# Kernel optimization log

Hardware: AMD Instinct MI355X
Metric: run time of the kernel (lower is better)

## Reference

```python
import jax, jax.numpy as jnp
import numpy as np

B, H, W, C = 2, 64, 64, 512
EPS = 1e-3  # keras BatchNormalization default epsilon


def _bn(x, g, b, m, v):
    # inference-mode batch norm over the last axis
    return (x - m) * jax.lax.rsqrt(v + EPS) * g + b


def setup_inputs() -> dict:
    key = jax.random.key(0)
    ks = jax.random.split(key, 12)
    C2 = C // 2

    def he(k, shape, fan_in):
        return jax.random.normal(k, shape, jnp.float32) * np.float32(np.sqrt(2.0 / fan_in))

    def bn_params(k, n):
        k1, k2, k3, k4 = jax.random.split(k, 4)
        g = 1.0 + 0.1 * jax.random.normal(k1, (n,), jnp.float32)
        b = 0.1 * jax.random.normal(k2, (n,), jnp.float32)
        m = 0.1 * jax.random.normal(k3, (n,), jnp.float32)
        v = jax.random.uniform(k4, (n,), jnp.float32, 0.5, 1.5)
        return g, b, m, v

    g1, b1, m1, v1 = bn_params(ks[1], 1)
    g2, b2, m2, v2 = bn_params(ks[2], C2)
    g3, b3, m3, v3 = bn_params(ks[3], C2)
    g4, b4, m4, v4 = bn_params(ks[4], 1)
    g5, b5, m5, v5 = bn_params(ks[5], C)

    return {
        "x": jax.random.normal(ks[0], (B, H, W, C), jnp.float32),
        # edge_aggregation_func: Dense(1) over the 4-neighbor axis
        "w_ea": he(ks[6], (4, 1), 4), "b_ea": jnp.zeros((1,), jnp.float32),
        "g1": g1, "b1": b1, "m1": m1, "v1": v1,
        # vertex_update_func: Dense(C//2) over 2C features
        "w_vu": he(ks[7], (2 * C, C2), 2 * C), "b_vu": jnp.zeros((C2,), jnp.float32),
        "g2": g2, "b2": b2, "m2": m2, "v2": v2,
        # edge_update_func: Dense(C//2) over 2C features
        "w_eu": he(ks[8], (2 * C, C2), 2 * C), "b_eu": jnp.zeros((C2,), jnp.float32),
        "g3": g3, "b3": b3, "m3": m3, "v3": v3,
        # update_edge_reduce_func: Dense(1) over the 4-neighbor axis
        "w_er": he(ks[9], (4, 1), 4), "b_er": jnp.zeros((1,), jnp.float32),
        "g4": g4, "b4": b4, "m4": m4, "v4": v4,
        # final 1x1 conv (no bias): [C + C//2, C]
        "w_fc": he(ks[10], (C + C2, C), C + C2),
        "g5": g5, "b5": b5, "m5": m5, "v5": v5,
    }


def reference(x, w_ea, b_ea, g1, b1, m1, v1,
              w_vu, b_vu, g2, b2, m2, v2,
              w_eu, b_eu, g3, b3, m3, v3,
              w_er, b_er, g4, b4, m4, v4,
              w_fc, g5, b5, m5, v5):
    # 4-neighbor cyclic-shift edges: [B,H,W,C,4] (H+1, H-1, W+1, W-1 rolls)
    neigh = jnp.stack([
        jnp.roll(x, 1, axis=1), jnp.roll(x, -1, axis=1),
        jnp.roll(x, 1, axis=2), jnp.roll(x, -1, axis=2)], axis=-1)
    edge = neigh * x[..., None]                                   # [B,H,W,C,4]

    # edge aggregation: Dense(1) over neighbor axis + BN(1) + ReLU
    agg = jax.nn.relu(_bn(jnp.einsum('bhwcn,no->bhwco', edge, w_ea) + b_ea,
                          g1, b1, m1, v1))[..., 0]                # [B,H,W,C]

    # vertex update: Dense(C/2) on concat([vertex, agg]) + BN + ReLU
    cat_v = jnp.concatenate([x, agg], axis=-1)                    # [B,H,W,2C]
    uv = jax.nn.relu(_bn(cat_v @ w_vu + b_vu, g2, b2, m2, v2))    # [B,H,W,C/2]

    # edge update: Dense(C/2) on concat([vertex x4, edge]) along channel
    vert4 = jnp.broadcast_to(x[..., None], edge.shape)            # [B,H,W,C,4]
    cat_e = jnp.concatenate([vert4, edge], axis=3)                # [B,H,W,2C,4]
    ue = jax.nn.relu(_bn(jnp.einsum('bhwcn,cd->bhwnd', cat_e, w_eu) + b_eu,
                         g3, b3, m3, v3))                          # [B,H,W,4,C/2]

    # reduce updated edges over neighbor axis: Dense(1) + BN(1) + ReLU
    ur = jax.nn.relu(_bn(jnp.einsum('bhwnd,no->bhwdo', ue, w_er) + b_er,
                         g4, b4, m4, v4))[..., 0]                 # [B,H,W,C/2]

    update_feature = uv * ur                                      # [B,H,W,C/2]

    # final aggregation: 1x1 conv (no bias) on concat([x, update]) + BN + ReLU
    out = jax.nn.relu(_bn(jnp.concatenate([x, update_feature], axis=-1) @ w_fc,
                          g5, b5, m5, v5))                         # [B,H,W,C]
    return out
```

## Files before the change

kernel.cpp:

```cpp
#include <hip/hip_runtime.h>
#include <stdint.h>


typedef __attribute__((ext_vector_type(8))) short bf16x8;
typedef __attribute__((ext_vector_type(4))) float f32x4;

#define EPS_BN 1e-3f

__device__ __forceinline__ short f2bf(float f) {
    union { float f; unsigned u; } cv;
    cv.f = f;
    unsigned r = cv.u + 0x7fffu + ((cv.u >> 16) & 1u);
    return (short)(r >> 16);
}
__device__ __forceinline__ float bf2f(short s) {
    union { unsigned u; float f; } cv;
    cv.u = ((unsigned)(unsigned short)s) << 16;
    return cv.f;
}


__device__ __forceinline__ void pack_one(const float* __restrict__ W, short* __restrict__ out,
                                         int K, int Ncol, int lb, int tid) {
    int i = lb * 256 + tid;
    int lane = i & 63, tile = i >> 6;
    int ktiles = K >> 5;
    int nt = tile / ktiles, kt = tile - nt * ktiles;
    int kbase = (kt << 5) + ((lane >> 4) << 3);
    int col = (nt << 4) + (lane & 15);
    bf16x8 v;
    #pragma unroll
    for (int j = 0; j < 8; ++j) v[j] = f2bf(W[(kbase + j) * Ncol + col]);
    ((bf16x8*)out)[(tile << 6) + lane] = v;
}

__global__ __launch_bounds__(256) void k_front(
    const float* __restrict__ x,
    const float* w_ea, const float* b_ea,
    const float* g1, const float* b1, const float* m1, const float* v1,
    const float* w_vu, const float* w_eu, const float* w_fc,
    const float* b_vu, const float* g2, const float* b2_, const float* m2, const float* v2,
    const float* b_eu, const float* g3, const float* b3, const float* m3, const float* v3,
    const float* w_er, const float* b_er,
    const float* g4, const float* b4, const float* m4, const float* v4,
    const float* g5, const float* b5, const float* m5, const float* v5,
    short* __restrict__ xb, short* __restrict__ agg,
    short* __restrict__ prodD, short* __restrict__ prodR,
    short* BpVu, short* BpEu, short* BpFc, float* P)
{
    int blk = blockIdx.x, t = threadIdx.x;
    if (blk >= 2048) {
        int b = blk - 2048;
        if (b < 128)      { pack_one(w_vu, BpVu, 1024, 256, b, t); }
        else if (b < 256) { pack_one(w_eu, BpEu, 1024, 256, b - 128, t); }
        else if (b < 448) { pack_one(w_fc, BpFc,  768, 512, b - 256, t); }
        else {
            for (int u = t; u < 512; u += 256) {
                float a5 = g5[u] * rsqrtf(v5[u] + EPS_BN);
                P[1032 + u] = a5;
                P[1544 + u] = b5[u] - m5[u] * a5;
            }
            {
                float a2 = g2[t] * rsqrtf(v2[t] + EPS_BN);
                P[8 + t]   = a2;
                P[264 + t] = (b_vu[t] - m2[t]) * a2 + b2_[t];
                float a3 = g3[t] * rsqrtf(v3[t] + EPS_BN);
                P[520 + t] = a3;
                P[776 + t] = (b_eu[t] - m3[t]) * a3 + b3[t];
            }
            if (t < 4) {
                P[2056 + t] = w_ea[t];
                P[2060 + t] = w_er[t];
            }
            if (t == 0) {
                float a4 = g4[0] * rsqrtf(v4[0] + EPS_BN);
                P[2] = a4;
                P[3] = (b_er[0] - m4[0]) * a4 + b4[0];
                float a1l = g1[0] * rsqrtf(v1[0] + EPS_BN);
                P[0] = a1l;
                P[1] = (b_ea[0] - m1[0]) * a1l + b1[0];
            }
        }
        return;
    }

    float a1 = g1[0] * rsqrtf(v1[0] + EPS_BN);
    float c1 = (b_ea[0] - m1[0]) * a1 + b1[0];
    float w0 = w_ea[0], w1 = w_ea[1], w2 = w_ea[2], w3 = w_ea[3];

    int idx = blk * 256 + t;
    int n = idx >> 6;
    int ci = idx & 63;
    int bh = n >> 6, h = bh & 63, w = n & 63;
    int bhb = bh & ~63;
    int rowU = ((bhb + ((h + 63) & 63)) << 6) + w;
    int rowD = ((bhb + ((h + 1) & 63)) << 6) + w;
    int rowL = (bh << 6) + ((w + 63) & 63);
    int rowR = (bh << 6) + ((w + 1) & 63);

    const f32x4* xv = (const f32x4*)x;
    int c4 = ci << 1;
    f32x4 vc[2], vU[2], vD[2], vL[2], vR[2];
    #pragma unroll
    for (int h2 = 0; h2 < 2; ++h2) {
        vc[h2] = xv[(n    << 7) + c4 + h2];
        vU[h2] = xv[(rowU << 7) + c4 + h2];
        vD[h2] = xv[(rowD << 7) + c4 + h2];
        vL[h2] = xv[(rowL << 7) + c4 + h2];
        vR[h2] = xv[(rowR << 7) + c4 + h2];
    }

    bf16x8 ob, xbv, pD, pR;
    #pragma unroll
    for (int h2 = 0; h2 < 2; ++h2) {
        #pragma unroll
        for (int j = 0; j < 4; ++j) {
            int e = h2 * 4 + j;
            float xc = vc[h2][j];
            float eU = xc * vU[h2][j], eD = xc * vD[h2][j];
            float eL = xc * vL[h2][j], eR = xc * vR[h2][j];
            float S = w0 * eU + w1 * eD + w2 * eL + w3 * eR;
            ob[e]  = f2bf(fmaxf(fmaf(a1, S, c1), 0.f));
            xbv[e] = f2bf(xc);
            pD[e] = f2bf(eD); pR[e] = f2bf(eR);
        }
    }
    int o = (n << 6) + ci;
    ((bf16x8*)agg)[o] = ob;
    ((bf16x8*)xb)[o] = xbv;
    ((bf16x8*)prodD)[o] = pD;
    ((bf16x8*)prodR)[o] = pR;
}

__global__ __launch_bounds__(256) void k_gemm_mid(
    const short* __restrict__ xb, const short* __restrict__ agg,
    const short* __restrict__ prodD, const short* __restrict__ prodR,
    const short* __restrict__ BpVu, const short* __restrict__ BpEu,
    const float* __restrict__ P,
    short* __restrict__ uvb, short* __restrict__ tvb,
    short* __restrict__ teDb, short* __restrict__ teRb)
{
    __shared__ __align__(16) short sA[2][32 * 64];
    int t = threadIdx.x, l = t & 63, w = t >> 6;
    int type = blockIdx.x & 3, rs = blockIdx.x >> 2;
    int r0 = rs << 5;

    const short* A0; const short* A1; int nchunk, ktbase;
    const bf16x8* Bp; short* Out;
    if (type == 0)      { A0 = xb;    A1 = agg;   nchunk = 16; Bp = (const bf16x8*)BpVu; ktbase = 0;  Out = uvb;  }
    else if (type == 1) { A0 = xb;    A1 = xb;    nchunk = 8;  Bp = (const bf16x8*)BpEu; ktbase = 0;  Out = tvb;  }
    else if (type == 2) { A0 = prodD; A1 = prodD; nchunk = 8;  Bp = (const bf16x8*)BpEu; ktbase = 16; Out = teDb; }
    else                { A0 = prodR; A1 = prodR; nchunk = 8;  Bp = (const bf16x8*)BpEu; ktbase = 16; Out = teRb; }

    int dr = t >> 3;
    int lcs = ((t & 7) ^ (dr & 7)) << 3;
    int srow = (r0 + dr) << 9;

    f32x4 acc[2][4];
    #pragma unroll
    for (int mi = 0; mi < 2; ++mi)
        #pragma unroll
        for (int nf = 0; nf < 4; ++nf) acc[mi][nf] = (f32x4){0.f, 0.f, 0.f, 0.f};

    bf16x8 g0 = *(const bf16x8*)(A0 + srow + lcs);

    int buf = 0;
    for (int kc = 0; kc < nchunk; ++kc) {
        ((bf16x8*)sA[buf])[t] = g0;
        __syncthreads();
        if (kc + 1 < nchunk) {
            int kn = kc + 1;
            const short* S = (kn < 8) ? A0 : A1;
            g0 = *(const bf16x8*)(S + srow + ((kn & 7) << 6) + lcs);
        }
        const short* Lb = sA[buf];
        #pragma unroll
        for (int kt = 0; kt < 2; ++kt) {
            bf16x8 af[2];
            #pragma unroll
            for (int mi = 0; mi < 2; ++mi) {
                int row = (mi << 4) + (l & 15);
                int lcolb = (kt << 6) + ((l >> 4) << 4);
                int addr = (row << 6) + ((lcolb ^ ((row & 7) << 4)) >> 1);
                af[mi] = *(const bf16x8*)(Lb + addr);
            }
            int kt32 = ktbase + (kc << 1) + kt;
            #pragma unroll
            for (int nf = 0; nf < 4; ++nf) {
                bf16x8 b = Bp[((((w << 2) + nf) << 5) + kt32) * 64 + l];
                #pragma unroll
                for (int mi = 0; mi < 2; ++mi)
                    acc[mi][nf] = __builtin_amdgcn_mfma_f32_16x16x32_bf16(af[mi], b, acc[mi][nf], 0, 0, 0);
            }
        }
        buf ^= 1;
    }

    #pragma unroll
    for (int nf = 0; nf < 4; ++nf) {
        int col = (w << 6) + (nf << 4) + (l & 15);
        float aa = P[8 + col], cc = P[264 + col];
        #pragma unroll
        for (int mi = 0; mi < 2; ++mi) {
            int rbase = r0 + (mi << 4) + ((l >> 4) << 2);
            #pragma unroll
            for (int j = 0; j < 4; ++j) {
                float v = acc[mi][nf][j];
                if (type == 0) v = fmaxf(fmaf(v, aa, cc), 0.f);
                Out[(rbase + j) * 256 + col] = f2bf(v);
            }
        }
    }
}

__global__ __launch_bounds__(256) void k_gemm_out(
    const short* __restrict__ xb,
    const short* __restrict__ tv, const short* __restrict__ teD,
    const short* __restrict__ teR, const short* __restrict__ uv,
    const short* __restrict__ BpFc, const float* __restrict__ P,
    float* __restrict__ out)
{
    __shared__ __align__(16) short sA[2][32 * 64];
    __shared__ __align__(16) short updL[4][32 * 64];
    int t = threadIdx.x, l = t & 63, w = t >> 6;
    int cq = blockIdx.x & 3, rs = blockIdx.x >> 2;
    int r0 = rs << 5;
    const bf16x8* Bp = (const bf16x8*)BpFc;

    int dr = t >> 3;
    int p8 = t & 7;
    int lcs = (p8 ^ (dr & 7)) << 3;

    {
        int n = r0 + dr;
        int bh = n >> 6, h = bh & 63, ww = n & 63;
        int bhb = bh & ~63;
        int nUp = ((bhb + ((h + 63) & 63)) << 6) + ww;
        int nLf = (bh << 6) + ((ww + 63) & 63);
        float w0 = P[2060], w1 = P[2061], w2 = P[2062], w3 = P[2063];
        float a4 = P[2], c4 = P[3];
        #pragma unroll
        for (int q = 0; q < 4; ++q) {
            int lc = (q << 6) + lcs;
            bf16x8 vTv = *(const bf16x8*)(tv  + n   * 256 + lc);
            bf16x8 vD  = *(const bf16x8*)(teD + n   * 256 + lc);
            bf16x8 vDu = *(const bf16x8*)(teD + nUp * 256 + lc);
            bf16x8 vR  = *(const bf16x8*)(teR + n   * 256 + lc);
            bf16x8 vRl = *(const bf16x8*)(teR + nLf * 256 + lc);
            bf16x8 vUv = *(const bf16x8*)(uv  + n   * 256 + lc);
            f32x4 a3a = *(const f32x4*)&P[520 + lc], a3b = *(const f32x4*)&P[524 + lc];
            f32x4 c3a = *(const f32x4*)&P[776 + lc], c3b = *(const f32x4*)&P[780 + lc];
            bf16x8 o;
            #pragma unroll
            for (int j = 0; j < 8; ++j) {
                float a3 = (j < 4) ? a3a[j & 3] : a3b[j & 3];
                float c3 = (j < 4) ? c3a[j & 3] : c3b[j & 3];
                float tvv = bf2f(vTv[j]);
                float ueU = fmaxf(fmaf(a3, tvv + bf2f(vDu[j]), c3), 0.f);
                float ueD = fmaxf(fmaf(a3, tvv + bf2f(vD[j]),  c3), 0.f);
                float ueL = fmaxf(fmaf(a3, tvv + bf2f(vRl[j]), c3), 0.f);
                float ueR = fmaxf(fmaf(a3, tvv + bf2f(vR[j]),  c3), 0.f);
                float s = w0 * ueU + w1 * ueD + w2 * ueL + w3 * ueR;
                float ur = fmaxf(fmaf(a4, s, c4), 0.f);
                o[j] = f2bf(ur * bf2f(vUv[j]));
            }
            *(bf16x8*)&updL[q][(dr << 6) + (p8 << 3)] = o;
        }
    }

    f32x4 acc[2][2];
    #pragma unroll
    for (int mi = 0; mi < 2; ++mi)
        #pragma unroll
        for (int nf = 0; nf < 2; ++nf) acc[mi][nf] = (f32x4){0.f, 0.f, 0.f, 0.f};

    bf16x8 g0 = *(const bf16x8*)(xb + ((r0 + dr) << 9) + lcs);
    int buf = 0;
    for (int kc = 0; kc < 12; ++kc) {
        const short* Lb;
        if (kc < 8) {
            ((bf16x8*)sA[buf])[t] = g0;
            __syncthreads();
            if (kc + 1 < 8)
                g0 = *(const bf16x8*)(xb + ((r0 + dr) << 9) + ((kc + 1) << 6) + lcs);
            Lb = sA[buf];
            buf ^= 1;
        } else {
            Lb = updL[kc - 8];
        }
        #pragma unroll
        for (int kt = 0; kt < 2; ++kt) {
            bf16x8 af[2];
            #pragma unroll
            for (int mi = 0; mi < 2; ++mi) {
                int row = (mi << 4) + (l & 15);
                int lcolb = (kt << 6) + ((l >> 4) << 4);
                int addr = (row << 6) + ((lcolb ^ ((row & 7) << 4)) >> 1);
                af[mi] = *(const bf16x8*)(Lb + addr);
            }
            #pragma unroll
            for (int nf = 0; nf < 2; ++nf) {
                int nt = (cq << 3) + (w << 1) + nf;
                bf16x8 b = Bp[(nt * 24 + (kc << 1) + kt) * 64 + l];
                #pragma unroll
                for (int mi = 0; mi < 2; ++mi)
                    acc[mi][nf] = __builtin_amdgcn_mfma_f32_16x16x32_bf16(af[mi], b, acc[mi][nf], 0, 0, 0);
            }
        }
    }

    #pragma unroll
    for (int nf = 0; nf < 2; ++nf) {
        int col = (cq << 7) + (w << 5) + (nf << 4) + (l & 15);
        float a5 = P[1032 + col], c5 = P[1544 + col];
        #pragma unroll
        for (int mi = 0; mi < 2; ++mi) {
            int rbase = r0 + (mi << 4) + ((l >> 4) << 2);
            #pragma unroll
            for (int j = 0; j < 4; ++j) {
                out[(rbase + j) * 512 + col] = fmaxf(fmaf(acc[mi][nf][j], a5, c5), 0.f);
            }
        }
    }
}

extern "C" void kernel_launch(void* const* d_in, const int* in_sizes, int n_in,
                              void* d_out, int out_size, void* d_ws, size_t ws_size,
                              hipStream_t stream)
{
    const float* x    = (const float*)d_in[0];
    const float* w_ea = (const float*)d_in[1];
    const float* b_ea = (const float*)d_in[2];
    const float* g1   = (const float*)d_in[3];
    const float* b1   = (const float*)d_in[4];
    const float* m1   = (const float*)d_in[5];
    const float* v1   = (const float*)d_in[6];
    const float* w_vu = (const float*)d_in[7];
    const float* b_vu = (const float*)d_in[8];
    const float* g2   = (const float*)d_in[9];
    const float* b2   = (const float*)d_in[10];
    const float* m2   = (const float*)d_in[11];
    const float* v2   = (const float*)d_in[12];
    const float* w_eu = (const float*)d_in[13];
    const float* b_eu = (const float*)d_in[14];
    const float* g3   = (const float*)d_in[15];
    const float* b3   = (const float*)d_in[16];
    const float* m3   = (const float*)d_in[17];
    const float* v3   = (const float*)d_in[18];
    const float* w_er = (const float*)d_in[19];
    const float* b_er = (const float*)d_in[20];
    const float* g4   = (const float*)d_in[21];
    const float* b4   = (const float*)d_in[22];
    const float* m4   = (const float*)d_in[23];
    const float* v4   = (const float*)d_in[24];
    const float* w_fc = (const float*)d_in[25];
    const float* g5   = (const float*)d_in[26];
    const float* b5   = (const float*)d_in[27];
    const float* m5   = (const float*)d_in[28];
    const float* v5   = (const float*)d_in[29];

    char* ws = (char*)d_ws;
    float* P = (float*)ws;
    size_t off = 16384;
    short* BpVu = (short*)(ws + off); off += (size_t)1024 * 256 * 2;
    short* BpEu = (short*)(ws + off); off += (size_t)1024 * 256 * 2;
    short* BpFc = (short*)(ws + off); off += (size_t)768 * 512 * 2;
    short* xbb  = (short*)(ws + off); off += (size_t)8192 * 512 * 2;
    short* aggb = (short*)(ws + off); off += (size_t)8192 * 512 * 2;
    short* prodD = (short*)(ws + off); off += (size_t)8192 * 512 * 2;
    short* prodR = (short*)(ws + off); off += (size_t)8192 * 512 * 2;
    short* uvb  = (short*)(ws + off); off += (size_t)8192 * 256 * 2;
    short* tvb  = (short*)(ws + off); off += (size_t)8192 * 256 * 2;
    short* teDb = (short*)(ws + off); off += (size_t)8192 * 256 * 2;
    short* teRb = (short*)(ws + off); off += (size_t)8192 * 256 * 2;

    k_front<<<2497, 256, 0, stream>>>(x, w_ea, b_ea, g1, b1, m1, v1,
                                      w_vu, w_eu, w_fc,
                                      b_vu, g2, b2, m2, v2,
                                      b_eu, g3, b3, m3, v3,
                                      w_er, b_er, g4, b4, m4, v4,
                                      g5, b5, m5, v5,
                                      xbb, aggb, prodD, prodR,
                                      BpVu, BpEu, BpFc, P);
    k_gemm_mid<<<1024, 256, 0, stream>>>(xbb, aggb, prodD, prodR, BpVu, BpEu, P,
                                         uvb, tvb, teDb, teRb);
    k_gemm_out<<<1024, 256, 0, stream>>>(xbb, tvb, teDb, teRb, uvb, BpFc, P,
                                         (float*)d_out);
}
```

Baseline: 69.68 us.

## Compute edge products on the fly in mid GEMM and enlarge GEMM tiles

The front kernel no longer writes the prodD/prodR edge-product tensors. The mid GEMM now recomputes them while staging A tiles, loading the shifted neighbor row of xb and multiplying in registers. Both GEMM kernels double their tile size (mid to 64 rows, out to 256 columns) and are unrolled into an explicit two-buffer pipeline, halving the grid. This removes about 16 MB of intermediate writes and reads and reuses each B fragment more often, at the cost of more registers, extra neighbor loads and products rounded from bf16 inputs.

```diff
diff --git a/kernel.cpp b/kernel.cpp
--- a/kernel.cpp
+++ b/kernel.cpp
@@ -45,7 +45,6 @@
     const float* g4, const float* b4, const float* m4, const float* v4,
     const float* g5, const float* b5, const float* m5, const float* v5,
     short* __restrict__ xb, short* __restrict__ agg,
-    short* __restrict__ prodD, short* __restrict__ prodR,
     short* BpVu, short* BpEu, short* BpFc, float* P)
 {
     int blk = blockIdx.x, t = threadIdx.x;
@@ -110,90 +109,118 @@
         vR[h2] = xv[(rowR << 7) + c4 + h2];
     }
 
-    bf16x8 ob, xbv, pD, pR;
+    bf16x8 ob, xbv;
     #pragma unroll
     for (int h2 = 0; h2 < 2; ++h2) {
         #pragma unroll
         for (int j = 0; j < 4; ++j) {
             int e = h2 * 4 + j;
             float xc = vc[h2][j];
-            float eU = xc * vU[h2][j], eD = xc * vD[h2][j];
-            float eL = xc * vL[h2][j], eR = xc * vR[h2][j];
-            float S = w0 * eU + w1 * eD + w2 * eL + w3 * eR;
+            float S = w0 * (xc * vU[h2][j]) + w1 * (xc * vD[h2][j])
+                    + w2 * (xc * vL[h2][j]) + w3 * (xc * vR[h2][j]);
             ob[e]  = f2bf(fmaxf(fmaf(a1, S, c1), 0.f));
             xbv[e] = f2bf(xc);
-            pD[e] = f2bf(eD); pR[e] = f2bf(eR);
         }
     }
     int o = (n << 6) + ci;
     ((bf16x8*)agg)[o] = ob;
     ((bf16x8*)xb)[o] = xbv;
-    ((bf16x8*)prodD)[o] = pD;
-    ((bf16x8*)prodR)[o] = pR;
-}
+}
+
+#define MID_LOAD(ga, gb, na_, nb_, kc) do {                                   \
+    const short* _S; int _off;                                                \
+    if (type == 0) { _S = ((kc) < 8) ? xb : agg; _off = ((kc) & 7) << 6; }    \
+    else           { _S = xb; _off = (kc) << 6; }                             \
+    ga = *(const bf16x8*)(_S + sAoff + _off + lcs);                           \
+    gb = *(const bf16x8*)(_S + sBoff + _off + lcs);                           \
+    if (type >= 2) {                                                          \
+        na_ = *(const bf16x8*)(xb + nAoff + _off + lcs);                      \
+        nb_ = *(const bf16x8*)(xb + nBoff + _off + lcs);                      \
+    }                                                                         \
+} while (0)
+
+#define MID_WRITE(slot, ga, gb, na_, nb_) do {                                \
+    bf16x8 _va = ga, _vb = gb;                                                \
+    if (type >= 2) {                                                          \
+        _Pragma("unroll") for (int _j = 0; _j < 8; ++_j) {                    \
+            _va[_j] = f2bf(bf2f(_va[_j]) * bf2f(na_[_j]));                    \
+            _vb[_j] = f2bf(bf2f(_vb[_j]) * bf2f(nb_[_j]));                    \
+        }                                                                     \
+    }                                                                         \
+    ((bf16x8*)sA[slot])[t] = _va;                                             \
+    ((bf16x8*)sA[slot])[256 + t] = _vb;                                       \
+} while (0)
+
+#define MID_COMPUTE(slot, kc) do {                                            \
+    const short* _Lb = sA[slot];                                              \
+    _Pragma("unroll") for (int _kt = 0; _kt < 2; ++_kt) {                     \
+        bf16x8 _af[4];                                                        \
+        _Pragma("unroll") for (int _mi = 0; _mi < 4; ++_mi) {                 \
+            int _row = (_mi << 4) + (l & 15);                                 \
+            int _lcolb = (_kt << 6) + ((l >> 4) << 4);                        \
+            int _addr = (_row << 6) + ((_lcolb ^ ((_row & 7) << 4)) >> 1);    \
+            _af[_mi] = *(const bf16x8*)(_Lb + _addr);                         \
+        }                                                                     \
+        int _kt32 = ktbase + ((kc) << 1) + _kt;                               \
+        _Pragma("unroll") for (int _nf = 0; _nf < 4; ++_nf) {                 \
+            bf16x8 _b = Bp[((((w << 2) + _nf) << 5) + _kt32) * 64 + l];       \
+            _Pragma("unroll") for (int _mi = 0; _mi < 4; ++_mi)               \
+                acc[_mi][_nf] = __builtin_amdgcn_mfma_f32_16x16x32_bf16(      \
+                    _af[_mi], _b, acc[_mi][_nf], 0, 0, 0);                    \
+        }                                                                     \
+    }                                                                         \
+} while (0)
 
 __global__ __launch_bounds__(256) void k_gemm_mid(
     const short* __restrict__ xb, const short* __restrict__ agg,
-    const short* __restrict__ prodD, const short* __restrict__ prodR,
     const short* __restrict__ BpVu, const short* __restrict__ BpEu,
     const float* __restrict__ P,
     short* __restrict__ uvb, short* __restrict__ tvb,
     short* __restrict__ teDb, short* __restrict__ teRb)
 {
-    __shared__ __align__(16) short sA[2][32 * 64];
+    __shared__ __align__(16) short sA[2][64 * 64];
     int t = threadIdx.x, l = t & 63, w = t >> 6;
     int type = blockIdx.x & 3, rs = blockIdx.x >> 2;
-    int r0 = rs << 5;
-
-    const short* A0; const short* A1; int nchunk, ktbase;
-    const bf16x8* Bp; short* Out;
-    if (type == 0)      { A0 = xb;    A1 = agg;   nchunk = 16; Bp = (const bf16x8*)BpVu; ktbase = 0;  Out = uvb;  }
-    else if (type == 1) { A0 = xb;    A1 = xb;    nchunk = 8;  Bp = (const bf16x8*)BpEu; ktbase = 0;  Out = tvb;  }
-    else if (type == 2) { A0 = prodD; A1 = prodD; nchunk = 8;  Bp = (const bf16x8*)BpEu; ktbase = 16; Out = teDb; }
-    else                { A0 = prodR; A1 = prodR; nchunk = 8;  Bp = (const bf16x8*)BpEu; ktbase = 16; Out = teRb; }
-
-    int dr = t >> 3;
-    int lcs = ((t & 7) ^ (dr & 7)) << 3;
-    int srow = (r0 + dr) << 9;
-
-    f32x4 acc[2][4];
-    #pragma unroll
-    for (int mi = 0; mi < 2; ++mi)
+    int r0 = rs << 6;
+    int dr = t >> 3, p8 = t & 7;
+    int lcs = (p8 ^ (dr & 7)) << 3;
+
+    int rA = r0 + dr, rB = r0 + dr + 32;
+    int nA = rA, nB = rB;
+    if (type == 2) {
+        int bhA = rA >> 6, bhB = rB >> 6;
+        nA = (((bhA & ~63) + (((bhA & 63) + 1) & 63)) << 6) + (rA & 63);
+        nB = (((bhB & ~63) + (((bhB & 63) + 1) & 63)) << 6) + (rB & 63);
+    } else if (type == 3) {
+        nA = (rA & ~63) + ((rA + 1) & 63);
+        nB = (rB & ~63) + ((rB + 1) & 63);
+    }
+    int sAoff = rA << 9, sBoff = rB << 9, nAoff = nA << 9, nBoff = nB << 9;
+
+    int nchunk = (type == 0) ? 16 : 8;
+    const bf16x8* Bp = (type == 0) ? (const bf16x8*)BpVu : (const bf16x8*)BpEu;
+    int ktbase = (type >= 2) ? 16 : 0;
+    short* Out = (type == 0) ? uvb : (type == 1) ? tvb : (type == 2) ? teDb : teRb;
+
+    f32x4 acc[4][4];
+    #pragma unroll
+    for (int mi = 0; mi < 4; ++mi)
         #pragma unroll
         for (int nf = 0; nf < 4; ++nf) acc[mi][nf] = (f32x4){0.f, 0.f, 0.f, 0.f};
 
-    bf16x8 g0 = *(const bf16x8*)(A0 + srow + lcs);
-
-    int buf = 0;
-    for (int kc = 0; kc < nchunk; ++kc) {
-        ((bf16x8*)sA[buf])[t] = g0;
+    bf16x8 gaA, gbA, naA, nbA, gaB, gbB, naB, nbB;
+    MID_LOAD(gaA, gbA, naA, nbA, 0);
+    MID_LOAD(gaB, gbB, naB, nbB, 1);
+
+    for (int kc2 = 0; kc2 < nchunk; kc2 += 2) {
+        MID_WRITE(0, gaA, gbA, naA, nbA);
         __syncthreads();
-        if (kc + 1 < nchunk) {
-            int kn = kc + 1;
-            const short* S = (kn < 8) ? A0 : A1;
-            g0 = *(const bf16x8*)(S + srow + ((kn & 7) << 6) + lcs);
-        }
-        const short* Lb = sA[buf];
-        #pragma unroll
-        for (int kt = 0; kt < 2; ++kt) {
-            bf16x8 af[2];
-            #pragma unroll
-            for (int mi = 0; mi < 2; ++mi) {
-                int row = (mi << 4) + (l & 15);
-                int lcolb = (kt << 6) + ((l >> 4) << 4);
-                int addr = (row << 6) + ((lcolb ^ ((row & 7) << 4)) >> 1);
-                af[mi] = *(const bf16x8*)(Lb + addr);
-            }
-            int kt32 = ktbase + (kc << 1) + kt;
-            #pragma unroll
-            for (int nf = 0; nf < 4; ++nf) {
-                bf16x8 b = Bp[((((w << 2) + nf) << 5) + kt32) * 64 + l];
-                #pragma unroll
-                for (int mi = 0; mi < 2; ++mi)
-                    acc[mi][nf] = __builtin_amdgcn_mfma_f32_16x16x32_bf16(af[mi], b, acc[mi][nf], 0, 0, 0);
-            }
-        }
-        buf ^= 1;
+        if (kc2 + 2 < nchunk) MID_LOAD(gaA, gbA, naA, nbA, kc2 + 2);
+        MID_COMPUTE(0, kc2);
+        MID_WRITE(1, gaB, gbB, naB, nbB);
+        __syncthreads();
+        if (kc2 + 3 < nchunk) MID_LOAD(gaB, gbB, naB, nbB, kc2 + 3);
+        MID_COMPUTE(1, kc2 + 1);
     }
 
     #pragma unroll
@@ -201,7 +228,7 @@
         int col = (w << 6) + (nf << 4) + (l & 15);
         float aa = P[8 + col], cc = P[264 + col];
         #pragma unroll
-        for (int mi = 0; mi < 2; ++mi) {
+        for (int mi = 0; mi < 4; ++mi) {
             int rbase = r0 + (mi << 4) + ((l >> 4) << 2);
             #pragma unroll
             for (int j = 0; j < 4; ++j) {
@@ -212,6 +239,25 @@
         }
     }
 }
+
+#define OUT_COMPUTE(Lb, kc) do {                                              \
+    _Pragma("unroll") for (int _kt = 0; _kt < 2; ++_kt) {                     \
+        bf16x8 _af[2];                                                        \
+        _Pragma("unroll") for (int _mi = 0; _mi < 2; ++_mi) {                 \
+            int _row = (_mi << 4) + (l & 15);                                 \
+            int _lcolb = (_kt << 6) + ((l >> 4) << 4);                        \
+            int _addr = (_row << 6) + ((_lcolb ^ ((_row & 7) << 4)) >> 1);    \
+            _af[_mi] = *(const bf16x8*)((Lb) + _addr);                        \
+        }                                                                     \
+        _Pragma("unroll") for (int _nf = 0; _nf < 4; ++_nf) {                 \
+            int _nt = (cg << 4) + (w << 2) + _nf;                             \
+            bf16x8 _b = Bp[(_nt * 24 + ((kc) << 1) + _kt) * 64 + l];          \
+            _Pragma("unroll") for (int _mi = 0; _mi < 2; ++_mi)               \
+                acc[_mi][_nf] = __builtin_amdgcn_mfma_f32_16x16x32_bf16(      \
+                    _af[_mi], _b, acc[_mi][_nf], 0, 0, 0);                    \
+        }                                                                     \
+    }                                                                         \
+} while (0)
 
 __global__ __launch_bounds__(256) void k_gemm_out(
     const short* __restrict__ xb,
@@ -220,16 +266,19 @@
     const short* __restrict__ BpFc, const float* __restrict__ P,
     float* __restrict__ out)
 {
-    __shared__ __align__(16) short sA[2][32 * 64];
+    __shared__ __align__(16) short sXb[2][32 * 64];
     __shared__ __align__(16) short updL[4][32 * 64];
     int t = threadIdx.x, l = t & 63, w = t >> 6;
-    int cq = blockIdx.x & 3, rs = blockIdx.x >> 2;
+    int cg = blockIdx.x & 1, rs = blockIdx.x >> 1;
     int r0 = rs << 5;
     const bf16x8* Bp = (const bf16x8*)BpFc;
 
-    int dr = t >> 3;
-    int p8 = t & 7;
+    int dr = t >> 3, p8 = t & 7;
     int lcs = (p8 ^ (dr & 7)) << 3;
+    int xrow = (r0 + dr) << 9;
+
+    bf16x8 gA = *(const bf16x8*)(xb + xrow + lcs);
+    bf16x8 gB = *(const bf16x8*)(xb + xrow + 64 + lcs);
 
     {
         int n = r0 + dr;
@@ -268,50 +317,28 @@
         }
     }
 
-    f32x4 acc[2][2];
+    f32x4 acc[2][4];
     #pragma unroll
     for (int mi = 0; mi < 2; ++mi)
         #pragma unroll
-        for (int nf = 0; nf < 2; ++nf) acc[mi][nf] = (f32x4){0.f, 0.f, 0.f, 0.f};
-
-    bf16x8 g0 = *(const bf16x8*)(xb + ((r0 + dr) << 9) + lcs);
-    int buf = 0;
-    for (int kc = 0; kc < 12; ++kc) {
-        const short* Lb;
-        if (kc < 8) {
-            ((bf16x8*)sA[buf])[t] = g0;
-            __syncthreads();
-            if (kc + 1 < 8)
-                g0 = *(const bf16x8*)(xb + ((r0 + dr) << 9) + ((kc + 1) << 6) + lcs);
-            Lb = sA[buf];
-            buf ^= 1;
-        } else {
-            Lb = updL[kc - 8];
-        }
-        #pragma unroll
-        for (int kt = 0; kt < 2; ++kt) {
-            bf16x8 af[2];
-            #pragma unroll
-            for (int mi = 0; mi < 2; ++mi) {
-                int row = (mi << 4) + (l & 15);
-                int lcolb = (kt << 6) + ((l >> 4) << 4);
-                int addr = (row << 6) + ((lcolb ^ ((row & 7) << 4)) >> 1);
-                af[mi] = *(const bf16x8*)(Lb + addr);
-            }
-            #pragma unroll
-            for (int nf = 0; nf < 2; ++nf) {
-                int nt = (cq << 3) + (w << 1) + nf;
-                bf16x8 b = Bp[(nt * 24 + (kc << 1) + kt) * 64 + l];
-                #pragma unroll
-                for (int mi = 0; mi < 2; ++mi)
-                    acc[mi][nf] = __builtin_amdgcn_mfma_f32_16x16x32_bf16(af[mi], b, acc[mi][nf], 0, 0, 0);
-            }
-        }
-    }
-
-    #pragma unroll
-    for (int nf = 0; nf < 2; ++nf) {
-        int col = (cq << 7) + (w << 5) + (nf << 4) + (l & 15);
+        for (int nf = 0; nf < 4; ++nf) acc[mi][nf] = (f32x4){0.f, 0.f, 0.f, 0.f};
+
+    for (int kc2 = 0; kc2 < 8; kc2 += 2) {
+        ((bf16x8*)sXb[0])[t] = gA;
+        __syncthreads();
+        if (kc2 + 2 < 8) gA = *(const bf16x8*)(xb + xrow + ((kc2 + 2) << 6) + lcs);
+        OUT_COMPUTE(sXb[0], kc2);
+        ((bf16x8*)sXb[1])[t] = gB;
+        __syncthreads();
+        if (kc2 + 3 < 8) gB = *(const bf16x8*)(xb + xrow + ((kc2 + 3) << 6) + lcs);
+        OUT_COMPUTE(sXb[1], kc2 + 1);
+    }
+    #pragma unroll
+    for (int ku = 0; ku < 4; ++ku) OUT_COMPUTE(updL[ku], 8 + ku);
+
+    #pragma unroll
+    for (int nf = 0; nf < 4; ++nf) {
+        int col = (cg << 8) + (w << 6) + (nf << 4) + (l & 15);
         float a5 = P[1032 + col], c5 = P[1544 + col];
         #pragma unroll
         for (int mi = 0; mi < 2; ++mi) {
@@ -367,8 +394,6 @@
     short* BpFc = (short*)(ws + off); off += (size_t)768 * 512 * 2;
     short* xbb  = (short*)(ws + off); off += (size_t)8192 * 512 * 2;
     short* aggb = (short*)(ws + off); off += (size_t)8192 * 512 * 2;
-    short* prodD = (short*)(ws + off); off += (size_t)8192 * 512 * 2;
-    short* prodR = (short*)(ws + off); off += (size_t)8192 * 512 * 2;
     short* uvb  = (short*)(ws + off); off += (size_t)8192 * 256 * 2;
     short* tvb  = (short*)(ws + off); off += (size_t)8192 * 256 * 2;
     short* teDb = (short*)(ws + off); off += (size_t)8192 * 256 * 2;
@@ -380,10 +405,9 @@
                                       b_eu, g3, b3, m3, v3,
                                       w_er, b_er, g4, b4, m4, v4,
                                       g5, b5, m5, v5,
-                                      xbb, aggb, prodD, prodR,
-                                      BpVu, BpEu, BpFc, P);
-    k_gemm_mid<<<1024, 256, 0, stream>>>(xbb, aggb, prodD, prodR, BpVu, BpEu, P,
-                                         uvb, tvb, teDb, teRb);
-    k_gemm_out<<<1024, 256, 0, stream>>>(xbb, tvb, teDb, teRb, uvb, BpFc, P,
-                                         (float*)d_out);
-}
+                                      xbb, aggb, BpVu, BpEu, BpFc, P);
+    k_gemm_mid<<<512, 256, 0, stream>>>(xbb, aggb, BpVu, BpEu, P,
+                                        uvb, tvb, teDb, teRb);
+    k_gemm_out<<<512, 256, 0, stream>>>(xbb, tvb, teDb, teRb, uvb, BpFc, P,
+                                        (float*)d_out);
+}
```

Result: slower. 85.15 us (+22.2%).
